# Kernel optimization log

Measured on AMD Instinct MI355X. Metric: run time of the kernel, lower is better.

## Reference

```python
import jax, jax.numpy as jnp
import numpy as np

WINDOW = (2, 7, 7)
DIM = 128
HEADS = 4
N = WINDOW[0] * WINDOW[1] * WINDOW[2]  # 98
TABLE = (2 * WINDOW[0] - 1) * (2 * WINDOW[1] - 1) * (2 * WINDOW[2] - 1)  # 507


def _rel_pos_index():
    d, h, w = WINDOW
    coords = np.stack(np.meshgrid(np.arange(d), np.arange(h), np.arange(w), indexing='ij'))  # [3,d,h,w]
    cf = coords.reshape(3, -1)  # [3, N]
    rel = cf[:, :, None] - cf[:, None, :]  # [3, N, N]
    rel = rel.transpose(1, 2, 0).copy()
    rel[:, :, 0] += d - 1
    rel[:, :, 1] += h - 1
    rel[:, :, 2] += w - 1
    rel[:, :, 0] *= (2 * h - 1) * (2 * w - 1)
    rel[:, :, 1] *= 2 * w - 1
    return jnp.asarray(rel.sum(-1), dtype=jnp.int32)  # [N, N]

REL_IDX = _rel_pos_index()


def setup_inputs() -> dict:
    key = jax.random.key(0)
    ks = jax.random.split(key, 8)
    B_, nW = 2048, 64
    x = jax.random.normal(ks[0], (B_, N, DIM), dtype=jnp.float32)
    mask = jax.random.normal(ks[1], (nW, N, N), dtype=jnp.float32)
    qkv_w = jax.random.normal(ks[2], (3 * DIM, DIM), dtype=jnp.float32) * (DIM ** -0.5)
    qkv_b = jnp.zeros((3 * DIM,), dtype=jnp.float32)
    rpb_table = jax.random.normal(ks[3], (TABLE, HEADS), dtype=jnp.float32) * 0.02
    proj_w = jax.random.normal(ks[4], (DIM, DIM), dtype=jnp.float32) * (DIM ** -0.5)
    proj_b = jnp.zeros((DIM,), dtype=jnp.float32)
    return {"x": x, "mask": mask, "qkv_w": qkv_w, "qkv_b": qkv_b,
            "rpb_table": rpb_table, "proj_w": proj_w, "proj_b": proj_b}


def reference(x, mask, qkv_w, qkv_b, rpb_table, proj_w, proj_b):
    B_, n, C = x.shape
    hd = C // HEADS
    scale = hd ** -0.5
    qkv = x @ qkv_w.T + qkv_b  # [B_, N, 3C]
    qkv = qkv.reshape(B_, n, 3, HEADS, hd).transpose(2, 0, 3, 1, 4)  # [3, B_, H, N, hd]
    q, k, v = qkv[0], qkv[1], qkv[2]
    attn = jnp.einsum('bhnd,bhmd->bhnm', q * scale, k)  # [B_, H, N, N]
    bias = rpb_table[REL_IDX.reshape(-1)].reshape(n, n, HEADS)  # gather
    attn = attn + bias.transpose(2, 0, 1)[None]  # [B_, H, N, N]
    nW = mask.shape[0]
    attn = attn.reshape(B_ // nW, nW, HEADS, n, n) + mask[None, :, None]
    attn = jax.nn.softmax(attn.reshape(B_, HEADS, n, n), axis=-1)
    out = jnp.einsum('bhnm,bhmd->bhnd', attn, v)  # [B_, H, N, hd]
    out = out.transpose(0, 2, 1, 3).reshape(B_, n, C)
    return out @ proj_w.T + proj_b
```

## Files before the change

### kernel.cpp

```cpp
#include <hip/hip_runtime.h>
#include <hip/hip_bf16.h>

#define NTOK 98
#define CDIM 128
#define SCALE 0.17677669529663687f
#define NEG_BIG -1e30f
#define CMBW 112

typedef short bf16x8 __attribute__((ext_vector_type(8)));
typedef short bf16x4 __attribute__((ext_vector_type(4)));
typedef float f32x4 __attribute__((ext_vector_type(4)));

#define MFMA32(a,b,c) __builtin_amdgcn_mfma_f32_16x16x32_bf16(a,b,c,0,0,0)

#if __has_builtin(__builtin_amdgcn_mfma_f32_16x16x16_bf16)
#define MFMA16(a,b,c) __builtin_amdgcn_mfma_f32_16x16x16_bf16(a,b,c,0,0,0)
#elif __has_builtin(__builtin_amdgcn_mfma_f32_16x16x16bf16_1k)
#define MFMA16(a,b,c) __builtin_amdgcn_mfma_f32_16x16x16bf16_1k(a,b,c,0,0,0)
#else
__device__ __forceinline__ f32x4 mfma16_asm(bf16x4 a, bf16x4 b, f32x4 c) {
  asm("v_mfma_f32_16x16x16_bf16 %0, %1, %2, %0" : "+v"(c) : "v"(a), "v"(b));
  return c;
}
#define MFMA16(a,b,c) mfma16_asm(a,b,c)
#endif

__device__ __forceinline__ unsigned short f2bf(float f) {
  __hip_bfloat16 h = __float2bfloat16(f);
  return __builtin_bit_cast(unsigned short, h);
}
__device__ __forceinline__ float bf2f(unsigned short b) {
  union { unsigned u; float f; } v; v.u = ((unsigned)b) << 16; return v.f;
}

__device__ __forceinline__ int swzK(int row, int col) {
  return row * 128 + (col ^ ((row & 7) << 3));
}

__device__ __forceinline__ bf16x8 ldfrag(const float* __restrict__ p) {
  float4 a = *(const float4*)p;
  float4 b = *(const float4*)(p + 4);
  bf16x8 fr;
  fr[0]=(short)f2bf(a.x); fr[1]=(short)f2bf(a.y); fr[2]=(short)f2bf(a.z); fr[3]=(short)f2bf(a.w);
  fr[4]=(short)f2bf(b.x); fr[5]=(short)f2bf(b.y); fr[6]=(short)f2bf(b.z); fr[7]=(short)f2bf(b.w);
  return fr;
}

__device__ __forceinline__ int pcode(int t) {
  int d = t / 49, r = t % 49;
  return d * 169 + (r / 7) * 13 + (r % 7);
}

__global__ __launch_bounds__(512)
void prep_w(const float* __restrict__ qkv_w, const float* __restrict__ qkv_b,
            const float* __restrict__ proj_w, const float* __restrict__ proj_b,
            unsigned short* __restrict__ qpre, unsigned short* __restrict__ ppre,
            float* __restrict__ bpre)
{
  int gid = blockIdx.x * 512 + threadIdx.x;
  if (gid < 6144) {
    int t = gid >> 8, rem = gid & 255, kk = rem >> 6, ln = rem & 63;
    int row = t * 16 + (ln & 15), col = kk * 32 + (ln >> 4) * 8;
    float sc = (row < CDIM) ? SCALE : 1.f;
    const float* s = qkv_w + (size_t)row * CDIM + col;
    unsigned short* d = qpre + (size_t)gid * 8;
#pragma unroll
    for (int e = 0; e < 8; ++e) d[e] = f2bf(s[e] * sc);
  } else if (gid < 8192) {
    int f2 = gid - 6144;
    int t = f2 >> 8, rem = f2 & 255, kk = rem >> 6, ln = rem & 63;
    const float* s = proj_w + (size_t)(t * 16 + (ln & 15)) * CDIM + kk * 32 + (ln >> 4) * 8;
    unsigned short* d = ppre + (size_t)f2 * 8;
#pragma unroll
    for (int e = 0; e < 8; ++e) d[e] = f2bf(s[e]);
  } else {
    int i = gid - 8192;
    if (i < 384) bpre[i] = qkv_b[i] * (i < CDIM ? SCALE : 1.f);
    else if (i < 512) bpre[i] = proj_b[i - 384];
  }
}

__global__ __launch_bounds__(256)
void prep_cmb(const float* __restrict__ mask, const float* __restrict__ rpb,
              float* __restrict__ cmb, int nW)
{
  const int total = 256 * NTOK * CMBW;
  for (int idx = blockIdx.x * 256 + threadIdx.x; idx < total; idx += gridDim.x * 256) {
    int row = idx / CMBW, n = idx - row * CMBW;
    int wh = row / NTOK, m = row - wh * NTOK;
    int w = wh >> 2, h = wh & 3;
    float v = NEG_BIG;
    if (n < NTOK)
      v = mask[((size_t)w * NTOK + m) * NTOK + n] + rpb[(pcode(m) - pcode(n) + 253) * 4 + h];
    cmb[idx] = v;
  }
}

template<bool PRE>
__global__ __launch_bounds__(512, 4)
void win_attn(const float* __restrict__ x, const float* __restrict__ mask,
              const float* __restrict__ qkv_w, const float* __restrict__ qkv_b,
              const float* __restrict__ rpb, const float* __restrict__ proj_w,
              const float* __restrict__ proj_b, float* __restrict__ out, int nW,
              const float* __restrict__ cmb, const unsigned short* __restrict__ qpre,
              const unsigned short* __restrict__ ppre, const float* __restrict__ bpre)
{
  __shared__ __align__(16) unsigned short xs[(PRE ? 112 : 98) * 128];
  __shared__ __align__(16) unsigned short kbuf[98 * 128];
  __shared__ __align__(16) unsigned short vbuf[128 * 100];
  __shared__ unsigned short rpbL[PRE ? 2 : 2028];
  __shared__ short mcode[PRE ? 2 : 112];

  const int tid = threadIdx.x;
  const int lane = tid & 63;
  const int wv = tid >> 6;
  const int lm = lane & 15;
  const int lg = lane >> 4;
  const int blk = blockIdx.x;
  const int wmod = blk % nW;
  const float* __restrict__ xblk = x + (size_t)blk * (NTOK * CDIM);
  const float* __restrict__ maskw = mask + (size_t)wmod * (NTOK * NTOK);

  if constexpr (!PRE) {
    if (tid < 112) mcode[tid] = (short)(tid < NTOK ? pcode(tid) : 0);
    for (int i = tid; i < 2028; i += 512) rpbL[i] = f2bf(rpb[i]);
  }
  for (int v = tid; v < NTOK * 32; v += 512) {
    int row = v >> 5, c4 = (v & 31) << 2;
    float4 f = *(const float4*)(xblk + row * CDIM + c4);
    uint2 u;
    u.x = (unsigned)f2bf(f.x) | ((unsigned)f2bf(f.y) << 16);
    u.y = (unsigned)f2bf(f.z) | ((unsigned)f2bf(f.w) << 16);
    *(uint2*)&xs[swzK(row, c4)] = u;
  }
  __syncthreads();

  auto wq = [&](int t, int kk) -> bf16x8 {
    if constexpr (PRE) return *(const bf16x8*)&qpre[(size_t)((t * 4 + kk) * 64 + lane) * 8];
    else return ldfrag(qkv_w + (size_t)(t * 16 + lm) * CDIM + kk * 32 + lg * 8);
  };

  {
    bf16x8 Bk[4], Bv[4];
#pragma unroll
    for (int kk = 0; kk < 4; ++kk) { Bk[kk] = wq(8 + wv, kk); Bv[kk] = wq(16 + wv, kk); }
    const float4 bk4 = *(const float4*)((PRE ? bpre : qkv_b) + CDIM + wv * 16 + lg * 4);
    const float  bv_ = (PRE ? bpre : qkv_b)[2 * CDIM + wv * 16 + lm];
    for (int mi = 0; mi < 7; ++mi) {
      int arow = mi * 16 + lm; if (arow > 97) arow = 97;
      bf16x8 A[4];
#pragma unroll
      for (int kk = 0; kk < 4; ++kk) A[kk] = *(const bf16x8*)&xs[swzK(arow, kk * 32 + lg * 8)];
      f32x4 ak = {0.f,0.f,0.f,0.f}, av = {0.f,0.f,0.f,0.f};
#pragma unroll
      for (int kk = 0; kk < 4; ++kk) {
        ak = MFMA32(Bk[kk], A[kk], ak);
        av = MFMA32(A[kk], Bv[kk], av);
      }
      int ktok = mi * 16 + lm;
      if (ktok < NTOK) {
        bf16x4 pk;
#pragma unroll
        for (int r = 0; r < 4; ++r) pk[r] = (short)f2bf(ak[r] + ((const float*)&bk4)[r]);
        *(bf16x4*)&kbuf[swzK(ktok, wv * 16 + lg * 4)] = pk;
      }
      int vtok0 = mi * 16 + lg * 4;
      if (vtok0 < 100) {
        bf16x4 pv;
#pragma unroll
        for (int r = 0; r < 4; ++r) pv[r] = (short)f2bf(av[r] + bv_);
        *(bf16x4*)&vbuf[(size_t)(wv * 16 + lm) * 100 + vtok0] = pv;
      }
    }
  }

  const bool have1 = (wv < 6);
  const int hh0 = wv / 7, mi0 = wv % 7;
  const int mi1 = wv + 1;

  bf16x4 bq[2][2][2];
#pragma unroll
  for (int j = 0; j < 2; ++j) {
    if (j == 0 || have1) {
      const int mi = j ? mi1 : mi0, hh = j ? 1 : hh0;
      int arow = mi * 16 + lm; if (arow > 97) arow = 97;
      bf16x8 Xf[4];
#pragma unroll
      for (int kk = 0; kk < 4; ++kk) Xf[kk] = *(const bf16x8*)&xs[swzK(arow, kk * 32 + lg * 8)];
#pragma unroll
      for (int g = 0; g < 2; ++g) {
        const int h = 2 * g + hh;
#pragma unroll
        for (int ct = 0; ct < 2; ++ct) {
          const int t = h * 2 + ct;
          f32x4 acc = {0.f,0.f,0.f,0.f};
#pragma unroll
          for (int kk = 0; kk < 4; ++kk) acc = MFMA32(wq(t, kk), Xf[kk], acc);
          const float4 qb4 = *(const float4*)((PRE ? bpre : qkv_b) + t * 16 + lg * 4);
#pragma unroll
          for (int r = 0; r < 4; ++r) {
            float vq = acc[r] + ((const float*)&qb4)[r];
            if constexpr (!PRE) vq *= SCALE;
            bq[j][g][ct][r] = (short)f2bf(vq);
          }
        }
      }
    }
  }
  __syncthreads();

#pragma unroll
  for (int g = 0; g < 2; ++g) {
#pragma unroll
    for (int j = 0; j < 2; ++j) {
      if (j == 0 || have1) {
        const int mi = j ? mi1 : mi0, hh = j ? 1 : hh0;
        const int h = 2 * g + hh, cb = h * 32;
        f32x4 s[7];
#pragma unroll
        for (int nj = 0; nj < 7; ++nj) {
          int krow = nj * 16 + lm; if (krow > 97) krow = 97;
          bf16x4 k0 = *(const bf16x4*)&kbuf[swzK(krow, cb + lg * 4)];
          bf16x4 k1 = *(const bf16x4*)&kbuf[swzK(krow, cb + 16 + lg * 4)];
          f32x4 z = {0.f,0.f,0.f,0.f};
          z = MFMA16(k0, bq[j][g][0], z);
          s[nj] = MFMA16(k1, bq[j][g][1], z);
        }
        const int m = mi * 16 + lm;
        const int mclamp = m > 97 ? 97 : m;
        float sum = 0.f;
        if constexpr (PRE) {
          const float* __restrict__ cp =
              cmb + ((size_t)(wmod * 4 + h) * NTOK + mclamp) * CMBW + lg * 4;
#pragma unroll
          for (int nj = 0; nj < 7; ++nj) {
            float4 cv = *(const float4*)(cp + nj * 16);
#pragma unroll
            for (int r = 0; r < 4; ++r) {
              float e = __expf(s[nj][r] + ((const float*)&cv)[r]);
              s[nj][r] = e; sum += e;
            }
          }
        } else {
          const int cm4 = ((int)mcode[mclamp]) * 4 + h + 1012;
          const float* __restrict__ mrow = maskw + mclamp * NTOK;
#pragma unroll
          for (int nj = 0; nj < 7; ++nj) {
            const int n0 = nj * 16 + lg * 4;
#pragma unroll
            for (int r = 0; r < 4; ++r) {
              int n = n0 + r;
              float val = NEG_BIG;
              if (n < NTOK) val = s[nj][r] + mrow[n] + bf2f(rpbL[cm4 - ((int)mcode[n]) * 4]);
              float e = __expf(val);
              s[nj][r] = e; sum += e;
            }
          }
        }
        sum += __shfl_xor(sum, 16);
        sum += __shfl_xor(sum, 32);
        const float inv = 1.f / sum;
        bf16x4 pp[7];
#pragma unroll
        for (int nj = 0; nj < 7; ++nj) {
#pragma unroll
          for (int r = 0; r < 4; ++r) pp[nj][r] = (short)f2bf(s[nj][r] * inv);
        }
#pragma unroll
        for (int dt = 0; dt < 2; ++dt) {
          const int d = cb + dt * 16 + lm;
          f32x4 acc = {0.f,0.f,0.f,0.f};
#pragma unroll
          for (int nj = 0; nj < 7; ++nj) {
            const int vc = nj < 6 ? nj * 16 + lg * 4 : 96;
            bf16x4 bv = *(const bf16x4*)&vbuf[(size_t)d * 100 + vc];
            acc = MFMA16(pp[nj], bv, acc);
          }
#pragma unroll
          for (int r = 0; r < 4; ++r) {
            int m2 = mi * 16 + lg * 4 + r;
            if (PRE || m2 < NTOK) xs[swzK(m2, d)] = f2bf(acc[r]);
          }
        }
      }
    }
  }
  __syncthreads();

  {
    bf16x8 Bp[4];
#pragma unroll
    for (int kk = 0; kk < 4; ++kk) {
      if constexpr (PRE) Bp[kk] = *(const bf16x8*)&ppre[(size_t)((wv * 4 + kk) * 64 + lane) * 8];
      else Bp[kk] = ldfrag(proj_w + (size_t)(wv * 16 + lm) * CDIM + kk * 32 + lg * 8);
    }
    const float4 pb4 = *(const float4*)((PRE ? bpre + 384 : proj_b) + wv * 16 + lg * 4);
    float* __restrict__ outb = out + (size_t)blk * (NTOK * CDIM);
    for (int mi = 0; mi < 7; ++mi) {
      int orow = mi * 16 + lm;
      if (!PRE && orow > 97) orow = 97;
      f32x4 acc = {0.f,0.f,0.f,0.f};
#pragma unroll
      for (int kk = 0; kk < 4; ++kk) {
        bf16x8 Bo = *(const bf16x8*)&xs[swzK(orow, kk * 32 + lg * 8)];
        acc = MFMA32(Bp[kk], Bo, acc);
      }
      int tok = mi * 16 + lm;
      if (tok < NTOK) {
        float4 o4;
        o4.x = acc[0] + pb4.x; o4.y = acc[1] + pb4.y;
        o4.z = acc[2] + pb4.z; o4.w = acc[3] + pb4.w;
        *(float4*)(outb + (size_t)tok * CDIM + wv * 16 + lg * 4) = o4;
      }
    }
  }
}

extern "C" void kernel_launch(void* const* d_in, const int* in_sizes, int n_in,
                              void* d_out, int out_size, void* d_ws, size_t ws_size,
                              hipStream_t stream) {
  const float* x      = (const float*)d_in[0];
  const float* mask   = (const float*)d_in[1];
  const float* qkv_w  = (const float*)d_in[2];
  const float* qkv_b  = (const float*)d_in[3];
  const float* rpb    = (const float*)d_in[4];
  const float* proj_w = (const float*)d_in[5];
  const float* proj_b = (const float*)d_in[6];
  int B  = in_sizes[0] / (NTOK * CDIM);
  int nW = in_sizes[1] / (NTOK * NTOK);

  const size_t CMB_B  = (size_t)256 * NTOK * CMBW * 4;
  const size_t QPRE_B = 24 * 4 * 64 * 8 * 2;
  const size_t PPRE_B = 8 * 4 * 64 * 8 * 2;
  const size_t BIAS_B = 512 * 4;
  const size_t need = CMB_B + QPRE_B + PPRE_B + BIAS_B;

  if (ws_size >= need) {
    float* cmb = (float*)d_ws;
    unsigned short* qpre = (unsigned short*)((char*)d_ws + CMB_B);
    unsigned short* ppre = (unsigned short*)((char*)d_ws + CMB_B + QPRE_B);
    float* bpre = (float*)((char*)d_ws + CMB_B + QPRE_B + PPRE_B);
    hipLaunchKernelGGL(prep_w, dim3(17), dim3(512), 0, stream,
                       qkv_w, qkv_b, proj_w, proj_b, qpre, ppre, bpre);
    hipLaunchKernelGGL(prep_cmb, dim3(1024), dim3(256), 0, stream, mask, rpb, cmb, nW);
    hipLaunchKernelGGL(win_attn<true>, dim3(B), dim3(512), 0, stream,
                       x, mask, qkv_w, qkv_b, rpb, proj_w, proj_b, (float*)d_out, nW,
                       cmb, qpre, ppre, bpre);
  } else {
    hipLaunchKernelGGL(win_attn<false>, dim3(B), dim3(512), 0, stream,
                       x, mask, qkv_w, qkv_b, rpb, proj_w, proj_b, (float*)d_out, nW,
                       (const float*)nullptr, (const unsigned short*)nullptr,
                       (const unsigned short*)nullptr, (const float*)nullptr);
  }
}
```

Before: 135.1 us.

## Use exp2 softmax, deferred normalization, packed bf16 converts and MFMA priority hints

Folds log2(e) into the Q scale and the precomputed mask+bias table so the softmax can use the hardware exp2 directly. Normalization moves from scaling every probability to scaling the PV output, using a fast reciprocal broadcast across lanes with shuffles. Scalar bf16 conversions are replaced by paired float2-to-bf16x2 converts. The QK^T products for both row blocks are computed before either softmax, and setprio hints are added around the MFMA sections. The trade-offs are slightly different rounding, because unnormalized probabilities are quantized to bf16, and more live registers from holding two score tiles at once.

Result: slower. 164.4 us (+21.7%).

```diff
diff --git a/kernel.cpp b/kernel.cpp
--- a/kernel.cpp
+++ b/kernel.cpp
@@ -4,6 +4,7 @@
 #define NTOK 98
 #define CDIM 128
 #define SCALE 0.17677669529663687f
+#define LOG2E 1.4426950408889634f
 #define NEG_BIG -1e30f
 #define CMBW 112
 
@@ -25,12 +26,33 @@
 #define MFMA16(a,b,c) mfma16_asm(a,b,c)
 #endif
 
+#if __has_builtin(__builtin_amdgcn_exp2f)
+#define EXP2F(x) __builtin_amdgcn_exp2f(x)
+#else
+#define EXP2F(x) exp2f(x)
+#endif
+#if __has_builtin(__builtin_amdgcn_rcpf)
+#define RCPF(x) __builtin_amdgcn_rcpf(x)
+#else
+#define RCPF(x) (1.f / (x))
+#endif
+
 __device__ __forceinline__ unsigned short f2bf(float f) {
   __hip_bfloat16 h = __float2bfloat16(f);
-  return __builtin_bit_cast(unsigned short, h);
+  unsigned short u;
+  __builtin_memcpy(&u, &h, 2);
+  return u;
 }
 __device__ __forceinline__ float bf2f(unsigned short b) {
   union { unsigned u; float f; } v; v.u = ((unsigned)b) << 16; return v.f;
+}
+__device__ __forceinline__ bf16x4 cvt4(f32x4 v) {
+  __hip_bfloat162 a = __float22bfloat162_rn(make_float2(v[0], v[1]));
+  __hip_bfloat162 b = __float22bfloat162_rn(make_float2(v[2], v[3]));
+  bf16x4 r;
+  __builtin_memcpy(&r, &a, 4);
+  __builtin_memcpy(((char*)&r) + 4, &b, 4);
+  return r;
 }
 
 __device__ __forceinline__ int swzK(int row, int col) {
@@ -61,7 +83,7 @@
   if (gid < 6144) {
     int t = gid >> 8, rem = gid & 255, kk = rem >> 6, ln = rem & 63;
     int row = t * 16 + (ln & 15), col = kk * 32 + (ln >> 4) * 8;
-    float sc = (row < CDIM) ? SCALE : 1.f;
+    float sc = (row < CDIM) ? SCALE * LOG2E : 1.f;
     const float* s = qkv_w + (size_t)row * CDIM + col;
     unsigned short* d = qpre + (size_t)gid * 8;
 #pragma unroll
@@ -75,7 +97,7 @@
     for (int e = 0; e < 8; ++e) d[e] = f2bf(s[e]);
   } else {
     int i = gid - 8192;
-    if (i < 384) bpre[i] = qkv_b[i] * (i < CDIM ? SCALE : 1.f);
+    if (i < 384) bpre[i] = qkv_b[i] * (i < CDIM ? SCALE * LOG2E : 1.f);
     else if (i < 512) bpre[i] = proj_b[i - 384];
   }
 }
@@ -91,7 +113,8 @@
     int w = wh >> 2, h = wh & 3;
     float v = NEG_BIG;
     if (n < NTOK)
-      v = mask[((size_t)w * NTOK + m) * NTOK + n] + rpb[(pcode(m) - pcode(n) + 253) * 4 + h];
+      v = (mask[((size_t)w * NTOK + m) * NTOK + n]
+           + rpb[(pcode(m) - pcode(n) + 253) * 4 + h]) * LOG2E;
     cmb[idx] = v;
   }
 }
@@ -128,10 +151,9 @@
   for (int v = tid; v < NTOK * 32; v += 512) {
     int row = v >> 5, c4 = (v & 31) << 2;
     float4 f = *(const float4*)(xblk + row * CDIM + c4);
-    uint2 u;
-    u.x = (unsigned)f2bf(f.x) | ((unsigned)f2bf(f.y) << 16);
-    u.y = (unsigned)f2bf(f.z) | ((unsigned)f2bf(f.w) << 16);
-    *(uint2*)&xs[swzK(row, c4)] = u;
+    f32x4 fv; fv[0]=f.x; fv[1]=f.y; fv[2]=f.z; fv[3]=f.w;
+    bf16x4 pk = cvt4(fv);
+    *(bf16x4*)&xs[swzK(row, c4)] = pk;
   }
   __syncthreads();
 
@@ -159,17 +181,17 @@
       }
       int ktok = mi * 16 + lm;
       if (ktok < NTOK) {
-        bf16x4 pk;
-#pragma unroll
-        for (int r = 0; r < 4; ++r) pk[r] = (short)f2bf(ak[r] + ((const float*)&bk4)[r]);
-        *(bf16x4*)&kbuf[swzK(ktok, wv * 16 + lg * 4)] = pk;
+        f32x4 t;
+#pragma unroll
+        for (int r = 0; r < 4; ++r) t[r] = ak[r] + ((const float*)&bk4)[r];
+        *(bf16x4*)&kbuf[swzK(ktok, wv * 16 + lg * 4)] = cvt4(t);
       }
       int vtok0 = mi * 16 + lg * 4;
       if (vtok0 < 100) {
-        bf16x4 pv;
-#pragma unroll
-        for (int r = 0; r < 4; ++r) pv[r] = (short)f2bf(av[r] + bv_);
-        *(bf16x4*)&vbuf[(size_t)(wv * 16 + lm) * 100 + vtok0] = pv;
+        f32x4 t;
+#pragma unroll
+        for (int r = 0; r < 4; ++r) t[r] = av[r] + bv_;
+        *(bf16x4*)&vbuf[(size_t)(wv * 16 + lm) * 100 + vtok0] = cvt4(t);
       }
     }
   }
@@ -197,12 +219,14 @@
 #pragma unroll
           for (int kk = 0; kk < 4; ++kk) acc = MFMA32(wq(t, kk), Xf[kk], acc);
           const float4 qb4 = *(const float4*)((PRE ? bpre : qkv_b) + t * 16 + lg * 4);
+          f32x4 tq;
 #pragma unroll
           for (int r = 0; r < 4; ++r) {
             float vq = acc[r] + ((const float*)&qb4)[r];
-            if constexpr (!PRE) vq *= SCALE;
-            bq[j][g][ct][r] = (short)f2bf(vq);
-          }
+            if constexpr (!PRE) vq *= SCALE * LOG2E;
+            tq[r] = vq;
+          }
+          bq[j][g][ct] = cvt4(tq);
         }
       }
     }
@@ -211,12 +235,12 @@
 
 #pragma unroll
   for (int g = 0; g < 2; ++g) {
+    f32x4 s[2][7];
 #pragma unroll
     for (int j = 0; j < 2; ++j) {
       if (j == 0 || have1) {
-        const int mi = j ? mi1 : mi0, hh = j ? 1 : hh0;
-        const int h = 2 * g + hh, cb = h * 32;
-        f32x4 s[7];
+        const int cb = (2 * g + (j ? 1 : hh0)) * 32;
+        __builtin_amdgcn_s_setprio(1);
 #pragma unroll
         for (int nj = 0; nj < 7; ++nj) {
           int krow = nj * 16 + lm; if (krow > 97) krow = 97;
@@ -224,8 +248,16 @@
           bf16x4 k1 = *(const bf16x4*)&kbuf[swzK(krow, cb + 16 + lg * 4)];
           f32x4 z = {0.f,0.f,0.f,0.f};
           z = MFMA16(k0, bq[j][g][0], z);
-          s[nj] = MFMA16(k1, bq[j][g][1], z);
+          s[j][nj] = MFMA16(k1, bq[j][g][1], z);
         }
+        __builtin_amdgcn_s_setprio(0);
+      }
+    }
+#pragma unroll
+    for (int j = 0; j < 2; ++j) {
+      if (j == 0 || have1) {
+        const int mi = j ? mi1 : mi0, hh = j ? 1 : hh0;
+        const int h = 2 * g + hh, cb = h * 32;
         const int m = mi * 16 + lm;
         const int mclamp = m > 97 ? 97 : m;
         float sum = 0.f;
@@ -237,8 +269,8 @@
             float4 cv = *(const float4*)(cp + nj * 16);
 #pragma unroll
             for (int r = 0; r < 4; ++r) {
-              float e = __expf(s[nj][r] + ((const float*)&cv)[r]);
-              s[nj][r] = e; sum += e;
+              float e = EXP2F(s[j][nj][r] + ((const float*)&cv)[r]);
+              s[j][nj][r] = e; sum += e;
             }
           }
         } else {
@@ -251,35 +283,38 @@
             for (int r = 0; r < 4; ++r) {
               int n = n0 + r;
               float val = NEG_BIG;
-              if (n < NTOK) val = s[nj][r] + mrow[n] + bf2f(rpbL[cm4 - ((int)mcode[n]) * 4]);
-              float e = __expf(val);
-              s[nj][r] = e; sum += e;
+              if (n < NTOK)
+                val = s[j][nj][r] + (mrow[n] + bf2f(rpbL[cm4 - ((int)mcode[n]) * 4])) * LOG2E;
+              float e = EXP2F(val);
+              s[j][nj][r] = e; sum += e;
             }
           }
         }
         sum += __shfl_xor(sum, 16);
         sum += __shfl_xor(sum, 32);
-        const float inv = 1.f / sum;
+        const float inv = RCPF(sum);
+        float invr[4];
+#pragma unroll
+        for (int r = 0; r < 4; ++r) invr[r] = __shfl(inv, lg * 4 + r);
         bf16x4 pp[7];
 #pragma unroll
-        for (int nj = 0; nj < 7; ++nj) {
-#pragma unroll
-          for (int r = 0; r < 4; ++r) pp[nj][r] = (short)f2bf(s[nj][r] * inv);
-        }
+        for (int nj = 0; nj < 7; ++nj) pp[nj] = cvt4(s[j][nj]);
 #pragma unroll
         for (int dt = 0; dt < 2; ++dt) {
           const int d = cb + dt * 16 + lm;
           f32x4 acc = {0.f,0.f,0.f,0.f};
+          __builtin_amdgcn_s_setprio(1);
 #pragma unroll
           for (int nj = 0; nj < 7; ++nj) {
             const int vc = nj < 6 ? nj * 16 + lg * 4 : 96;
             bf16x4 bv = *(const bf16x4*)&vbuf[(size_t)d * 100 + vc];
             acc = MFMA16(pp[nj], bv, acc);
           }
+          __builtin_amdgcn_s_setprio(0);
 #pragma unroll
           for (int r = 0; r < 4; ++r) {
             int m2 = mi * 16 + lg * 4 + r;
-            if (PRE || m2 < NTOK) xs[swzK(m2, d)] = f2bf(acc[r]);
+            if (PRE || m2 < NTOK) xs[swzK(m2, d)] = f2bf(acc[r] * invr[r]);
           }
         }
       }
```
